# Kernel optimization log

Measured on AMD Instinct MI355X. Metric: run time of the kernel, lower is better.

The kernel has to match this reference:

```python
import jax, jax.numpy as jnp
import numpy as np

N_ATOMS = 512
N_FEATURES = 64
BATCH = 8
BINS = 64
SEG_LEN = 1
LEAKY_SLOPE = 0.01


def _segments(n, length=1):
    # all pairs of segments (i,i+length),(j,j+length), i<j, excluding end1==start2
    n_seg = n - length
    i, j = np.triu_indices(n_seg, k=1)
    seg = np.stack([i, i + length, j, j + length], axis=1)
    return seg[seg[:, 1] != seg[:, 2]].astype(np.int32)


def _nnorm(v):
    return v / jnp.linalg.norm(v, axis=-1, keepdims=True)


def _writhe(segments, xyz):
    # segments: (P,4) int, xyz: (B,N,3) -> (B,P)
    smat = xyz[:, segments]                                  # (B,P,4,3)
    B, P = smat.shape[0], smat.shape[1]
    # displacements r02,r03,r12,r13 (point a in seg1 -> point b in seg2)
    disp = _nnorm((smat[:, :, None, 2:, :] - smat[:, :, :2, None, :]).reshape(B, P, 4, 3))
    idx_a = jnp.array([0, 1, 3, 2])
    idx_b = jnp.array([1, 3, 2, 0])
    crosses = _nnorm(jnp.cross(disp[:, :, idx_a], disp[:, :, idx_b]))
    dots = jnp.clip(jnp.sum(crosses * crosses[:, :, idx_b], axis=-1), -1.0, 1.0)
    omega = jnp.arcsin(dots).sum(-1)                         # (B,P)
    signs = jnp.sign(jnp.sum(
        jnp.cross(_nnorm(smat[:, :, 3] - smat[:, :, 2]), _nnorm(smat[:, :, 1] - smat[:, :, 0]))
        * disp[:, :, 0], axis=-1))
    return omega * signs / (2.0 * jnp.pi)


def _rbf(x, start=-1.0, end=1.0, number=BINS):
    # soft_one_hot_linspace, basis='gaussian', cutoff=False
    values = jnp.linspace(start, end, number, dtype=x.dtype)
    step = values[1] - values[0]
    diff = (x[..., None] - values) / step
    return jnp.exp(-(diff ** 2)) / 1.12


def setup_inputs() -> dict:
    key = jax.random.key(0)
    k = jax.random.split(key, 4)
    seg = jnp.asarray(_segments(N_ATOMS, SEG_LEN))           # (129795,4)
    return {
        "x": jax.random.normal(k[0], (BATCH, N_ATOMS, N_FEATURES), jnp.float32),
        "xyz": jax.random.normal(k[1], (BATCH, N_ATOMS, 3), jnp.float32) * 3.0,
        "segments": seg,
        "W1": jax.random.normal(k[2], (BINS, N_FEATURES), jnp.float32) / np.sqrt(BINS),
        "b1": jnp.zeros((N_FEATURES,), jnp.float32),
        "W2": jax.random.normal(k[3], (N_FEATURES, N_FEATURES), jnp.float32) / np.sqrt(N_FEATURES),
        "b2": jnp.zeros((N_FEATURES,), jnp.float32),
    }


def reference(x, xyz, segments, W1, b1, W2, b2):
    wr = _writhe(segments, xyz)                              # (B,P)
    # bidirectional edges between segment start points
    src = jnp.concatenate([segments[:, 0], segments[:, 2]])  # (E,)
    dst = jnp.concatenate([segments[:, 2], segments[:, 0]])  # (E,)
    wr_e = jnp.concatenate([wr, wr], axis=1)                 # (B,E)
    h = jax.nn.leaky_relu(_rbf(wr_e) @ W1 + b1, LEAKY_SLOPE) # (B,E,F)
    msg = (h @ W2 + b2) * x[:, src]                          # (B,E,F)
    agg = jax.vmap(lambda m: jax.ops.segment_sum(m, dst, num_segments=N_ATOMS))(msg)
    return x + agg                                           # residual update (B,N,F)
```

## Files before the change

kernel.cpp:

```cpp
#include <hip/hip_runtime.h>
#include <hip/hip_bf16.h>
#include <math.h>
#include <stdint.h>

#define N_ATOMS 512
#define NF 64
#define NB 8
#define NBINS 64
#define NSEG 511
#define NTF 8192
#define NSENT 2554

__device__ __forceinline__ float dot3(float ax, float ay, float az,
                                      float bx, float by, float bz) {
    return fmaf(ax, bx, fmaf(ay, by, az * bz));
}

__device__ __forceinline__ uint16_t bf16_bits(float f) {
    union { __hip_bfloat16 h; uint16_t u; } cv;
    cv.h = __float2bfloat16(f);
    return cv.u;
}

__device__ __forceinline__ float compute_wr(const float* __restrict__ pb, int i, int j) {
    float p0x = pb[3*i+0], p0y = pb[3*i+1], p0z = pb[3*i+2];
    float p1x = pb[3*i+3], p1y = pb[3*i+4], p1z = pb[3*i+5];
    float p2x = pb[3*j+0], p2y = pb[3*j+1], p2z = pb[3*j+2];
    float p3x = pb[3*j+3], p3y = pb[3*j+4], p3z = pb[3*j+5];

    float d0x = p2x-p0x, d0y = p2y-p0y, d0z = p2z-p0z;
    float d1x = p3x-p0x, d1y = p3y-p0y, d1z = p3z-p0z;
    float d2x = p2x-p1x, d2y = p2y-p1y, d2z = p2z-p1z;
    float d3x = p3x-p1x, d3y = p3y-p1y, d3z = p3z-p1z;
    {
        float n0 = rsqrtf(dot3(d0x,d0y,d0z,d0x,d0y,d0z)); d0x*=n0; d0y*=n0; d0z*=n0;
        float n1 = rsqrtf(dot3(d1x,d1y,d1z,d1x,d1y,d1z)); d1x*=n1; d1y*=n1; d1z*=n1;
        float n2 = rsqrtf(dot3(d2x,d2y,d2z,d2x,d2y,d2z)); d2x*=n2; d2y*=n2; d2z*=n2;
        float n3 = rsqrtf(dot3(d3x,d3y,d3z,d3x,d3y,d3z)); d3x*=n3; d3y*=n3; d3z*=n3;
    }
    float c0x = d0y*d1z - d0z*d1y, c0y = d0z*d1x - d0x*d1z, c0z = d0x*d1y - d0y*d1x;
    float c1x = d1y*d3z - d1z*d3y, c1y = d1z*d3x - d1x*d3z, c1z = d1x*d3y - d1y*d3x;
    float c3x = d2y*d0z - d2z*d0y, c3y = d2z*d0x - d2x*d0z, c3z = d2x*d0y - d2y*d0x;
    {
        float n0 = rsqrtf(dot3(c0x,c0y,c0z,c0x,c0y,c0z)); c0x*=n0; c0y*=n0; c0z*=n0;
        float n1 = rsqrtf(dot3(c1x,c1y,c1z,c1x,c1y,c1z)); c1x*=n1; c1y*=n1; c1z*=n1;
        float n3 = rsqrtf(dot3(c3x,c3y,c3z,c3x,c3y,c3z)); c3x*=n3; c3y*=n3; c3z*=n3;
    }
    float t0 = fminf(fmaxf(dot3(c0x,c0y,c0z, c1x,c1y,c1z), -1.f), 1.f);
    float t1 = fminf(fmaxf(dot3(c1x,c1y,c1z, c3x,c3y,c3z), -1.f), 1.f);
    float t3 = fminf(fmaxf(dot3(c3x,c3y,c3z, c0x,c0y,c0z), -1.f), 1.f);
    float omega = asinf(t0) + asinf(t1) + asinf(t3) + 1.5707963267948966f;
    float ex = p3x-p2x, ey = p3y-p2y, ez = p3z-p2z;
    float fx = p1x-p0x, fy = p1y-p0y, fz = p1z-p0z;
    float gx = ey*fz - ez*fy, gy = ez*fx - ex*fz, gz = ex*fy - ey*fx;
    float sgd = dot3(gx,gy,gz, d0x,d0y,d0z);
    float sgn = (sgd > 0.f) ? 1.f : ((sgd < 0.f) ? -1.f : 0.f);
    return omega * sgn * 0.15915494309189535f;
}

__launch_bounds__(256)
__global__ void prepass(
        const float* __restrict__ xyz, const int* __restrict__ seg,
        const float* __restrict__ x, float* __restrict__ out,
        const float* __restrict__ W1, const float* __restrict__ b1,
        const float* __restrict__ W2, const float* __restrict__ b2,
        uint16_t* __restrict__ tabh, uint32_t* __restrict__ ta, int P) {
    __shared__ float lh[4][64];

    if (blockIdx.x < NTF / 4) {
        const int widx = threadIdx.x >> 6;
        const int lane = threadIdx.x & 63;
        const int g = blockIdx.x * 4 + widx;

        float wr = -1.0f + (2.0f / (float)(NTF - 1)) * (float)g;
        float tt = (wr + 1.0f) * 31.5f;

        float h0 = 0.f, h1 = 0.f, h2 = 0.f, h3 = 0.f;
        #pragma unroll
        for (int k = 0; k < NBINS; k += 4) {
            float d0 = tt - (float)(k + 0);
            float d1 = tt - (float)(k + 1);
            float d2 = tt - (float)(k + 2);
            float d3 = tt - (float)(k + 3);
            h0 = fmaf(__expf(-d0 * d0) * 0.8928571428571429f, W1[(k + 0) * NF + lane], h0);
            h1 = fmaf(__expf(-d1 * d1) * 0.8928571428571429f, W1[(k + 1) * NF + lane], h1);
            h2 = fmaf(__expf(-d2 * d2) * 0.8928571428571429f, W1[(k + 2) * NF + lane], h2);
            h3 = fmaf(__expf(-d3 * d3) * 0.8928571428571429f, W1[(k + 3) * NF + lane], h3);
        }
        float h = ((h0 + h1) + (h2 + h3)) + b1[lane];
        h = fmaxf(h, 0.01f * h);
        lh[widx][lane] = h;
        __syncthreads();

        float m0 = 0.f, m1 = 0.f, m2 = 0.f, m3 = 0.f;
        #pragma unroll
        for (int k = 0; k < NF; k += 4) {
            m0 = fmaf(lh[widx][k + 0], W2[(k + 0) * NF + lane], m0);
            m1 = fmaf(lh[widx][k + 1], W2[(k + 1) * NF + lane], m1);
            m2 = fmaf(lh[widx][k + 2], W2[(k + 2) * NF + lane], m2);
            m3 = fmaf(lh[widx][k + 3], W2[(k + 3) * NF + lane], m3);
        }
        float m = ((m0 + m1) + (m2 + m3)) + b2[lane];
        tabh[g * NF + lane] = bf16_bits(m);
        if (g == 0) tabh[NTF * NF + lane] = 0;
    } else {
        const int tid2 = (blockIdx.x - NTF / 4) * 256 + threadIdx.x;

        if (tid2 < NB * N_ATOMS * NF) out[tid2] = x[tid2];

        if (tid2 < NB * P) {
            const int b = tid2 / P;
            const int e = tid2 - b * P;
            int4 sv = ((const int4*)seg)[e];
            const int i = sv.x;
            const int j = sv.z;

            float w  = compute_wr(xyz + b * (N_ATOMS * 3), i, j);
            float tf = (w + 1.0f) * ((float)(NTF - 1) * 0.5f);
            tf = fminf(fmaxf(tf, 0.0f), (float)(NTF - 1));
            int t0 = (int)(tf + 0.5f);
            t0 = (t0 > NTF - 1) ? (NTF - 1) : t0;
            uint32_t u = (uint32_t)t0 << 6;

            ta[(b << 18) + (i << 9) + j] = u;
            ta[(b << 18) + (j << 9) + i] = u;
        } else if (tid2 < NB * P + NB * NSENT) {
            const int idx = tid2 - NB * P;
            const int b = idx / NSENT;
            const int k = idx - b * NSENT;
            int d, s;
            if      (k < 512)  { d = k;        s = k;     }
            else if (k < 1023) { d = k - 512;  s = d + 1; }
            else if (k < 1534) { s = k - 1023; d = s + 1; }
            else if (k < 2044) { d = k - 1534; s = NSEG;  }
            else               { s = k - 2044; d = NSEG;  }
            ta[(b << 18) + (d << 9) + s] = (uint32_t)NTF << 6;
        }
    }
}

__launch_bounds__(256)
__global__ void agg8(
        const float* __restrict__ x, const uint32_t* __restrict__ ta,
        const uint16_t* __restrict__ tabh, float* __restrict__ out) {
    __shared__ float lds_x[4096];

    const int widx = threadIdx.x >> 6;
    const int lane = threadIdx.x & 63;
    const int bid = blockIdx.x;
    const int c    = bid & 7;
    const int dgrp = (bid >> 3) & 127;
    const int b    = bid >> 10;
    const int dst  = dgrp * 4 + widx;

    const float* xc = x + ((size_t)b << 15) + (c << 12);
    #pragma unroll
    for (int k = 0; k < 16; ++k)
        lds_x[k * 256 + threadIdx.x] = xc[k * 256 + threadIdx.x];
    __syncthreads();

    if (dst < NSEG) {
        const int tav = (int)ta[((size_t)b << 18) + (dst << 9) + (c << 6) + lane];

        float acc = 0.0f;
        #pragma unroll
        for (int ee = 0; ee < 64; ++ee) {
            const int off = __builtin_amdgcn_readlane(tav, ee);
            const float mv = __uint_as_float((uint32_t)tabh[off + lane] << 16);
            acc = fmaf(mv, lds_x[(ee << 6) + lane], acc);
        }
        atomicAdd(&out[((size_t)b << 15) + (dst << 6) + lane], acc);
    }
}


__global__ void init_out_kernel(const float* __restrict__ x, float* __restrict__ out, int n) {
    int idx = blockIdx.x * blockDim.x + threadIdx.x;
    if (idx < n) out[idx] = x[idx];
}

__device__ __forceinline__ void compute_m(
        const float* __restrict__ pb, int i, int j,
        const float* __restrict__ W1, const float* __restrict__ b1,
        const float* __restrict__ W2, const float* __restrict__ b2,
        float* __restrict__ mout) {
    float wr = compute_wr(pb, i, j);
    float acc_[NBINS];
    {
        float tt = (wr + 1.0f) * 31.5f;
        #pragma unroll
        for (int k = 0; k < NBINS; ++k) {
            float d = tt - (float)k;
            acc_[k] = __expf(-d * d) * 0.8928571428571429f;
        }
    }
    float h_[NF];
    #pragma unroll
    for (int f = 0; f < NF; ++f) h_[f] = b1[f];
    #pragma unroll
    for (int k = 0; k < NBINS; ++k) {
        float r = acc_[k];
        #pragma unroll
        for (int f = 0; f < NF; ++f) h_[f] = fmaf(r, W1[k * NF + f], h_[f]);
    }
    #pragma unroll
    for (int f = 0; f < NF; ++f) h_[f] = fmaxf(h_[f], 0.01f * h_[f]);
    #pragma unroll
    for (int f = 0; f < NF; ++f) acc_[f] = b2[f];
    #pragma unroll
    for (int k = 0; k < NF; ++k) {
        float hk = h_[k];
        #pragma unroll
        for (int f = 0; f < NF; ++f) acc_[f] = fmaf(hk, W2[k * NF + f], acc_[f]);
    }
    #pragma unroll
    for (int f = 0; f < NF; ++f) mout[f] = acc_[f];
}

__launch_bounds__(256, 2)
__global__ void writhe_msg_atomic_kernel(
        const float* __restrict__ x, const float* __restrict__ xyz,
        const int* __restrict__ seg,
        const float* __restrict__ W1, const float* __restrict__ b1,
        const float* __restrict__ W2, const float* __restrict__ b2,
        float* __restrict__ out, int P, int n_tiles) {
    __shared__ __hip_bfloat16 lds_m[4][64 * 65];
    __shared__ int lds_i[4][64];
    __shared__ int lds_j[4][64];

    const int widx = threadIdx.x >> 6;
    const int lane = threadIdx.x & 63;
    const int wave_g = blockIdx.x * 4 + widx;
    const int b = wave_g / n_tiles;
    const int tile = wave_g - b * n_tiles;
    const int bc = (b < NB) ? b : 0;
    const int e = tile * 64 + lane;
    const bool valid = (b < NB) && (e < P);

    int4 sv = valid ? ((const int4*)seg)[e] : make_int4(0, 1, 2, 3);
    const int i = sv.x;
    const int j = sv.z;

    float m[NF];
    compute_m(xyz + bc * (N_ATOMS * 3), i, j, W1, b1, W2, b2, m);

    const float scale = valid ? 1.0f : 0.0f;
    #pragma unroll
    for (int f = 0; f < NF; ++f)
        lds_m[widx][lane * 65 + f] = __float2bfloat16(m[f] * scale);
    lds_i[widx][lane] = i;
    lds_j[widx][lane] = j;
    __syncthreads();

    const float* xb = x + bc * (N_ATOMS * NF);
    float* ob = out + bc * (N_ATOMS * NF);
    int cur_i = lds_i[widx][0];
    float acc_i = 0.0f;
    for (int ee = 0; ee < 64; ++ee) {
        int ie = lds_i[widx][ee];
        int je = lds_j[widx][ee];
        float mv = __bfloat162float(lds_m[widx][ee * 65 + lane]);
        float xi = xb[ie * NF + lane];
        float xj = xb[je * NF + lane];
        atomicAdd(&ob[je * NF + lane], mv * xi);
        if (ie != cur_i) {
            atomicAdd(&ob[cur_i * NF + lane], acc_i);
            acc_i = 0.0f;
            cur_i = ie;
        }
        acc_i = fmaf(mv, xj, acc_i);
    }
    atomicAdd(&ob[cur_i * NF + lane], acc_i);
}

extern "C" void kernel_launch(void* const* d_in, const int* in_sizes, int n_in,
                              void* d_out, int out_size, void* d_ws, size_t ws_size,
                              hipStream_t stream) {
    const float* x   = (const float*)d_in[0];
    const float* xyz = (const float*)d_in[1];
    const int*   seg = (const int*)d_in[2];
    const float* W1  = (const float*)d_in[3];
    const float* b1  = (const float*)d_in[4];
    const float* W2  = (const float*)d_in[5];
    const float* b2  = (const float*)d_in[6];
    float* out = (float*)d_out;

    const int P = in_sizes[2] / 4;
    const int n_tiles = (P + 63) / 64;

    const size_t tabh_bytes = (size_t)(NTF + 1) * NF * sizeof(uint16_t);
    const size_t ta_bytes   = (size_t)NB * N_ATOMS * N_ATOMS * sizeof(uint32_t);
    const size_t need_ws = tabh_bytes + ta_bytes;

    if (ws_size >= need_ws) {
        uint16_t* tabh = (uint16_t*)d_ws;
        uint32_t* ta   = (uint32_t*)((char*)d_ws + tabh_bytes);

        const int nbuild = NTF / 4;
        const int npass_th = NB * P + NB * NSENT;
        const int npass = (npass_th + 255) / 256;
        hipLaunchKernelGGL(prepass, dim3(nbuild + npass), dim3(256), 0, stream,
                           xyz, seg, x, out, W1, b1, W2, b2, tabh, ta, P);

        hipLaunchKernelGGL(agg8, dim3(NB * 128 * 8), dim3(256), 0, stream,
                           x, ta, tabh, out);
    } else {
        const int n = out_size;
        hipLaunchKernelGGL(init_out_kernel, dim3((n + 255) / 256), dim3(256), 0, stream,
                           x, out, n);
        const int total_waves = NB * n_tiles;
        const int blocks = (total_waves + 3) / 4;
        hipLaunchKernelGGL(writhe_msg_atomic_kernel, dim3(blocks), dim3(256), 0, stream,
                           x, xyz, seg, W1, b1, W2, b2, out, P, n_tiles);
    }
}
```

Measured before the change: 113.4 us.

## Stage per-batch coordinates in LDS and widen aggregation blocks to eight waves

The prepass now tiles edges per batch and loads that batch's xyz coordinates into shared memory, so the writhe calculation reads positions from LDS instead of gathering them from global memory. The x-to-out copy and the sentinel writes get their own dedicated block ranges. The aggregation kernel uses 512-thread blocks covering eight destinations, which halves how often each x chunk is reloaded into LDS. The price is more LDS per block in the prepass, a fixed tile count that requires a guard on P, and larger blocks that may reduce occupancy.

```diff
diff --git a/kernel.cpp b/kernel.cpp
--- a/kernel.cpp
+++ b/kernel.cpp
@@ -10,6 +10,7 @@
 #define NSEG 511
 #define NTF 8192
 #define NSENT 2554
+#define ETILES 508
 
 __device__ __forceinline__ float dot3(float ax, float ay, float az,
                                       float bx, float by, float bz) {
@@ -22,7 +23,7 @@
     return cv.u;
 }
 
-__device__ __forceinline__ float compute_wr(const float* __restrict__ pb, int i, int j) {
+__device__ __forceinline__ float compute_wr(const float* pb, int i, int j) {
     float p0x = pb[3*i+0], p0y = pb[3*i+1], p0z = pb[3*i+2];
     float p1x = pb[3*i+3], p1y = pb[3*i+4], p1z = pb[3*i+5];
     float p2x = pb[3*j+0], p2y = pb[3*j+1], p2z = pb[3*j+2];
@@ -65,12 +66,14 @@
         const float* __restrict__ W1, const float* __restrict__ b1,
         const float* __restrict__ W2, const float* __restrict__ b2,
         uint16_t* __restrict__ tabh, uint32_t* __restrict__ ta, int P) {
-    __shared__ float lh[4][64];
-
-    if (blockIdx.x < NTF / 4) {
+    __shared__ float lds[1536];
+
+    const unsigned bx = blockIdx.x;
+
+    if (bx < NTF / 4) {
         const int widx = threadIdx.x >> 6;
         const int lane = threadIdx.x & 63;
-        const int g = blockIdx.x * 4 + widx;
+        const int g = bx * 4 + widx;
 
         float wr = -1.0f + (2.0f / (float)(NTF - 1)) * (float)g;
         float tt = (wr + 1.0f) * 31.5f;
@@ -89,33 +92,38 @@
         }
         float h = ((h0 + h1) + (h2 + h3)) + b1[lane];
         h = fmaxf(h, 0.01f * h);
-        lh[widx][lane] = h;
+        lds[widx * 64 + lane] = h;
         __syncthreads();
 
         float m0 = 0.f, m1 = 0.f, m2 = 0.f, m3 = 0.f;
         #pragma unroll
         for (int k = 0; k < NF; k += 4) {
-            m0 = fmaf(lh[widx][k + 0], W2[(k + 0) * NF + lane], m0);
-            m1 = fmaf(lh[widx][k + 1], W2[(k + 1) * NF + lane], m1);
-            m2 = fmaf(lh[widx][k + 2], W2[(k + 2) * NF + lane], m2);
-            m3 = fmaf(lh[widx][k + 3], W2[(k + 3) * NF + lane], m3);
+            m0 = fmaf(lds[widx * 64 + k + 0], W2[(k + 0) * NF + lane], m0);
+            m1 = fmaf(lds[widx * 64 + k + 1], W2[(k + 1) * NF + lane], m1);
+            m2 = fmaf(lds[widx * 64 + k + 2], W2[(k + 2) * NF + lane], m2);
+            m3 = fmaf(lds[widx * 64 + k + 3], W2[(k + 3) * NF + lane], m3);
         }
         float m = ((m0 + m1) + (m2 + m3)) + b2[lane];
         tabh[g * NF + lane] = bf16_bits(m);
         if (g == 0) tabh[NTF * NF + lane] = 0;
-    } else {
-        const int tid2 = (blockIdx.x - NTF / 4) * 256 + threadIdx.x;
-
-        if (tid2 < NB * N_ATOMS * NF) out[tid2] = x[tid2];
-
-        if (tid2 < NB * P) {
-            const int b = tid2 / P;
-            const int e = tid2 - b * P;
+    } else if (bx < NTF / 4 + NB * ETILES) {
+        const int rel = bx - NTF / 4;
+        const int b = rel / ETILES;
+        const int tile = rel - b * ETILES;
+
+        const float* xb = xyz + b * (N_ATOMS * 3);
+        #pragma unroll
+        for (int k = 0; k < 6; ++k)
+            lds[k * 256 + threadIdx.x] = xb[k * 256 + threadIdx.x];
+        __syncthreads();
+
+        const int e = tile * 256 + threadIdx.x;
+        if (e < P) {
             int4 sv = ((const int4*)seg)[e];
             const int i = sv.x;
             const int j = sv.z;
 
-            float w  = compute_wr(xyz + b * (N_ATOMS * 3), i, j);
+            float w  = compute_wr(lds, i, j);
             float tf = (w + 1.0f) * ((float)(NTF - 1) * 0.5f);
             tf = fminf(fmaxf(tf, 0.0f), (float)(NTF - 1));
             int t0 = (int)(tf + 0.5f);
@@ -124,8 +132,13 @@
 
             ta[(b << 18) + (i << 9) + j] = u;
             ta[(b << 18) + (j << 9) + i] = u;
-        } else if (tid2 < NB * P + NB * NSENT) {
-            const int idx = tid2 - NB * P;
+        }
+    } else if (bx < NTF / 4 + NB * ETILES + 1024) {
+        const int tid = (bx - (NTF / 4 + NB * ETILES)) * 256 + threadIdx.x;
+        out[tid] = x[tid];
+    } else {
+        const int idx = (bx - (NTF / 4 + NB * ETILES + 1024)) * 256 + threadIdx.x;
+        if (idx < NB * NSENT) {
             const int b = idx / NSENT;
             const int k = idx - b * NSENT;
             int d, s;
@@ -139,8 +152,8 @@
     }
 }
 
-__launch_bounds__(256)
-__global__ void agg8(
+__launch_bounds__(512)
+__global__ void agg9(
         const float* __restrict__ x, const uint32_t* __restrict__ ta,
         const uint16_t* __restrict__ tabh, float* __restrict__ out) {
     __shared__ float lds_x[4096];
@@ -149,14 +162,14 @@
     const int lane = threadIdx.x & 63;
     const int bid = blockIdx.x;
     const int c    = bid & 7;
-    const int dgrp = (bid >> 3) & 127;
-    const int b    = bid >> 10;
-    const int dst  = dgrp * 4 + widx;
+    const int dgrp = (bid >> 3) & 63;
+    const int b    = bid >> 9;
+    const int dst  = dgrp * 8 + widx;
 
     const float* xc = x + ((size_t)b << 15) + (c << 12);
     #pragma unroll
-    for (int k = 0; k < 16; ++k)
-        lds_x[k * 256 + threadIdx.x] = xc[k * 256 + threadIdx.x];
+    for (int k = 0; k < 8; ++k)
+        lds_x[k * 512 + threadIdx.x] = xc[k * 512 + threadIdx.x];
     __syncthreads();
 
     if (dst < NSEG) {
@@ -292,17 +305,16 @@
     const size_t ta_bytes   = (size_t)NB * N_ATOMS * N_ATOMS * sizeof(uint32_t);
     const size_t need_ws = tabh_bytes + ta_bytes;
 
-    if (ws_size >= need_ws) {
+    if (ws_size >= need_ws && P <= ETILES * 256) {
         uint16_t* tabh = (uint16_t*)d_ws;
         uint32_t* ta   = (uint32_t*)((char*)d_ws + tabh_bytes);
 
-        const int nbuild = NTF / 4;
-        const int npass_th = NB * P + NB * NSENT;
-        const int npass = (npass_th + 255) / 256;
-        hipLaunchKernelGGL(prepass, dim3(nbuild + npass), dim3(256), 0, stream,
+        const int nsent_blocks = (NB * NSENT + 255) / 256;
+        const int total_blocks = NTF / 4 + NB * ETILES + 1024 + nsent_blocks;
+        hipLaunchKernelGGL(prepass, dim3(total_blocks), dim3(256), 0, stream,
                            xyz, seg, x, out, W1, b1, W2, b2, tabh, ta, P);
 
-        hipLaunchKernelGGL(agg8, dim3(NB * 128 * 8), dim3(256), 0, stream,
+        hipLaunchKernelGGL(agg9, dim3(NB * 64 * 8), dim3(512), 0, stream,
                            x, ta, tabh, out);
     } else {
         const int n = out_size;
```

After: 111.0 us. 1.02x faster.
